# Optimization experiments

Hardware: AMD Instinct MI355X
Metric: run time of the kernel (lower is better)

The kernel has to match this reference:

```python
import jax, jax.numpy as jnp
import numpy as np

LMAX = 5
RESOLUTION = 12
ASPECT_RATIO = 2
BATCH = 256
NB = 2 * RESOLUTION                       # res_beta = 24
NA = round(2 * ASPECT_RATIO * RESOLUTION)  # res_alpha = res_gamma = 48
DIM = sum((2 * l + 1) ** 2 for l in range(LMAX + 1))  # 286

# normalize2mom constant for tanh: (E_{z~N(0,1)}[tanh(z)^2])^{-1/2}
_x = np.linspace(-12.0, 12.0, 1_000_001)
_pdf = np.exp(-0.5 * _x * _x) / np.sqrt(2.0 * np.pi)
ACT_CST = float(np.trapz(np.tanh(_x) ** 2 * _pdf, _x) ** -0.5)  # ~1.5927


def _su2_generators(j):
    m = np.arange(-j, j)
    raising = np.diag(-np.sqrt(j * (j + 1) - m * (m + 1)), k=-1).astype(complex)
    m = np.arange(-j + 1, j + 1)
    lowering = np.diag(np.sqrt(j * (j + 1) - m * (m - 1)), k=1).astype(complex)
    m = np.arange(-j, j + 1)
    return np.stack([0.5 * (raising + lowering), np.diag(1j * m), -0.5j * (raising - lowering)])


def _q_real_to_complex(l):
    q = np.zeros((2 * l + 1, 2 * l + 1), dtype=complex)
    for m in range(-l, 0):
        q[l + m, l + abs(m)] = 1 / np.sqrt(2)
        q[l + m, l - abs(m)] = -1j / np.sqrt(2)
    q[l, l] = 1
    for m in range(1, l + 1):
        q[l + m, l + abs(m)] = (-1) ** m / np.sqrt(2)
        q[l + m, l - abs(m)] = 1j * (-1) ** m / np.sqrt(2)
    return (-1j) ** l * q


def _so3_generators(l):
    X = _su2_generators(l)
    Q = _q_real_to_complex(l)
    return np.real(np.conj(Q.T)[None] @ X @ Q[None])  # real [3, 2l+1, 2l+1]


def _expm_angles(A, t):
    """exp(t_n * A) for real antisymmetric A via eigendecomposition. -> [n, d, d] real"""
    vals, vecs = np.linalg.eig(A.astype(complex))
    inv = np.linalg.inv(vecs)
    phases = np.exp(t[:, None] * vals[None, :])  # [n, d]
    return np.real(np.einsum('ij,nj,jk->nik', vecs, phases, inv))


def _build_D_and_qw():
    # Euler angle grids (e3nn SO3Grid convention)
    b = (np.arange(NB) + 0.5) / NB * np.pi          # beta   [nb]
    a = np.arange(NA) / NA * 2.0 * np.pi            # alpha=gamma [na]
    blocks = []
    for l in range(LMAX + 1):
        X = _so3_generators(l)
        Ra = _expm_angles(X[1], a)   # exp(alpha * X1)  [na,d,d]
        Rb = _expm_angles(X[0], b)   # exp(beta  * X0)  [nb,d,d]
        # D^l(a,b,c) = Ra[a] @ Rb[b] @ Ra[c]
        Dl = np.einsum('xij,yjk,zkl->xyzil', Ra, Rb, Ra)
        blocks.append(np.sqrt(2 * l + 1) * Dl.reshape(NA, NB, NA, -1))
    D = np.concatenate(blocks, axis=-1).astype(np.float32)  # [na, nb, na, dim]
    # lie_learn / Kostelec-Rockmore quadrature weights for beta
    bb = NB // 2
    k = np.arange(bb)
    j = np.arange(2 * bb)
    w = (2.0 / bb) * np.sin(np.pi * (2 * j + 1) / (4.0 * bb)) * np.sum(
        (1.0 / (2 * k + 1))[None, :]
        * np.sin((2 * j[:, None] + 1) * (2 * k[None, :] + 1) * np.pi / (4.0 * bb)),
        axis=1,
    )
    w = w / (2.0 * (2 * bb) ** 2)
    qw = (w * NB ** 2 / NA ** 2).astype(np.float32)  # [nb]
    return jnp.asarray(D), jnp.asarray(qw)


def setup_inputs() -> dict:
    key = jax.random.key(0)
    features = jax.random.normal(key, (BATCH, DIM), dtype=jnp.float32)
    D, qw = _build_D_and_qw()
    return {"features": features, "D": D, "qw": qw}


def reference(features, D, qw):
    dim = D.shape[-1]
    s = jnp.sqrt(jnp.asarray(dim, features.dtype))
    # to_grid: [B, dim] x [na, nb, na, dim] -> [B, na, nb, na]
    g = jnp.einsum('bi,xyzi->bxyz', features, D) / s
    # normalized pointwise nonlinearity on SO(3) samples
    g = ACT_CST * jnp.tanh(g)
    # from_grid: quadrature-weighted projection back onto flat Wigner basis
    return jnp.einsum('bxyz,y,xyzi->bi', g, qw, D) * s
```

## Files before the change

kernel.cpp:

```cpp
#include <hip/hip_runtime.h>
#include <hip/hip_bf16.h>

#define DIM    286
#define DIMP   288
#define NBATCH 256
#define NB_    24
#define NA_    48
#define ZC     32
#define NTILES 1728
#define NCHUNK 256
#define S_CONST 16.911534525287763f
#define INV_S   0.05913123959890826f
#define ACT_CST 1.5927f
#define TWO_LOG2E 2.8853900817779268f

typedef short bf16x8 __attribute__((ext_vector_type(8)));
typedef float f32x4  __attribute__((ext_vector_type(4)));

#define WS_FBF  0u
#define WS_PART 147456u

typedef const __attribute__((address_space(1))) char GA;
typedef __attribute__((address_space(3))) char LA;
__device__ __forceinline__ void gload_lds16(const void* g, void* l) {
    __builtin_amdgcn_global_load_lds((GA*)g, (LA*)l, 16, 0, 0);
}

__global__ void k_prepF(const float* __restrict__ F, __hip_bfloat16* __restrict__ Fbf) {
    int o = blockIdx.x * 256 + threadIdx.x;
    int row = o / DIMP, col = o % DIMP;
    float v = (col < DIM) ? F[row * DIM + col] * INV_S : 0.f;
    Fbf[o] = __float2bfloat16(v);
}

__launch_bounds__(512, 2)
__global__ void k_main(const __hip_bfloat16* __restrict__ Fbf,
                       const float* __restrict__ D,
                       const float* __restrict__ qw,
                       __hip_bfloat16* __restrict__ part) {
    __shared__ __align__(16) float Traw[2][9216];
    __shared__ __align__(16) char DsB[18432];
    __shared__ __align__(16) char DtB[18432];
    __shared__ __align__(16) char GsB[16384];
    __shared__ float qs[24];

    int t = threadIdx.x;
    int wave = t >> 6, lane = t & 63, ln = lane & 15, q = lane >> 4;
    int cA = (ln * 64 + q * 16) ^ ((ln & 7) << 4);
    int rq = ln * 64 + q * 16;
    int gA0 = (wave << 11) + (rq ^ ((ln >> 2) << 4));
    int gA1 = (wave << 11) + 1024 + (rq ^ ((4 + (ln >> 2)) << 4));

    if (t < 24) qs[t] = qw[t] * S_CONST;

    int rowbase = wave * 32;
    const __hip_bfloat16* fp0 = Fbf + (size_t)(rowbase + ln) * DIMP + q * 8;
    const __hip_bfloat16* fp1 = fp0 + 16 * DIMP;

    f32x4 acc[2][18];
    #pragma unroll
    for (int h = 0; h < 2; ++h)
        #pragma unroll
        for (int n = 0; n < 18; ++n) acc[h][n] = (f32x4){0.f, 0.f, 0.f, 0.f};

    int bx = blockIdx.x;
    int tstart = (bx < 192) ? bx * 7 : bx * 6 + 192;
    int ntile = (bx < 192) ? 7 : 6;

    int zseed = t / 144, iseed = t % 144;

    #define STAGE(TI, BUF) do {                                                    \
        const char* _s = (const char*)(D + (size_t)(tstart + (TI)) * 9152);        \
        char* _d = (char*)Traw[BUF];                                               \
        _Pragma("unroll")                                                          \
        for (int _j = 0; _j < 5; ++_j) {                                           \
            int _c = wave + _j * 8;                                                \
            if (_c < 35 || (_c == 35 && lane < 48))                                \
                gload_lds16(_s + _c * 1024 + lane * 16, _d + _c * 1024);           \
        }                                                                          \
    } while (0)

    STAGE(0, 0);
    STAGE(1, 1);
    asm volatile("s_waitcnt lgkmcnt(0)" ::: "memory");

    #pragma unroll 1
    for (int k = 0; k < ntile; ++k) {
        if (k + 1 < ntile) {
            if (wave < 4) asm volatile("s_waitcnt vmcnt(5)" ::: "memory");
            else          asm volatile("s_waitcnt vmcnt(4)" ::: "memory");
        } else {
            asm volatile("s_waitcnt vmcnt(0)" ::: "memory");
        }
        __builtin_amdgcn_s_barrier();

        const float* T = Traw[k & 1];
        {
            int zz = zseed, ii = iseed;
            #pragma unroll
            for (int m = 0; m < 9; ++m) {
                int i = ii * 2;
                __hip_bfloat162 o2;
                if (i < DIM) {
                    float2 v = *(const float2*)(&T[zz * DIM + i]);
                    o2.x = __float2bfloat16(v.x); o2.y = __float2bfloat16(v.y);
                } else {
                    o2.x = __float2bfloat16(0.f); o2.y = o2.x;
                }
                int off = (((i >> 5) * 2048) + zz * 64 + (i & 31) * 2) ^ ((zz & 7) << 4);
                *(__hip_bfloat162*)(DsB + off) = o2;
                zz += 3; ii += 80;
                if (ii >= 144) { ii -= 144; ++zz; }
            }
        }
        #pragma unroll
        for (int s5 = 0; s5 < 3; ++s5) {
            int idx = t + s5 * 512;
            if (idx < 1152) {
                int i = idx >> 2, zc = idx & 3;
                __hip_bfloat16 o8[8];
                #pragma unroll
                for (int j = 0; j < 8; ++j)
                    o8[j] = __float2bfloat16(T[(zc * 8 + j) * DIM + i]);
                int off = (i * 64 + zc * 16) ^ ((i & 7) << 4);
                *(bf16x8*)(DtB + off) = *(const bf16x8*)o8;
            }
        }
        asm volatile("s_waitcnt lgkmcnt(0)" ::: "memory");
        __builtin_amdgcn_s_barrier();

        if (k + 2 < ntile) STAGE(k + 2, k & 1);

        int z0t = (tstart + k) * 32;
        float qv0 = qs[((z0t + ln) / 48) % 24];
        float qv1 = qs[((z0t + 16 + ln) / 48) % 24];

        f32x4 g00 = (f32x4){0.f,0.f,0.f,0.f}, g01 = (f32x4){0.f,0.f,0.f,0.f};
        f32x4 g10 = (f32x4){0.f,0.f,0.f,0.f}, g11 = (f32x4){0.f,0.f,0.f,0.f};
        #pragma unroll 3
        for (int ks = 0; ks < 9; ++ks) {
            bf16x8 a0 = *(const bf16x8*)(fp0 + ks * 32);
            bf16x8 a1 = *(const bf16x8*)(fp1 + ks * 32);
            bf16x8 b0 = *(const bf16x8*)(DsB + ks * 2048 + cA);
            bf16x8 b1 = *(const bf16x8*)(DsB + ks * 2048 + 1024 + cA);
            g00 = __builtin_amdgcn_mfma_f32_16x16x32_bf16(a0, b0, g00, 0, 0, 0);
            g01 = __builtin_amdgcn_mfma_f32_16x16x32_bf16(a0, b1, g01, 0, 0, 0);
            g10 = __builtin_amdgcn_mfma_f32_16x16x32_bf16(a1, b0, g10, 0, 0, 0);
            g11 = __builtin_amdgcn_mfma_f32_16x16x32_bf16(a1, b1, g11, 0, 0, 0);
        }
        #pragma unroll
        for (int h = 0; h < 2; ++h) {
            #pragma unroll
            for (int zh = 0; zh < 2; ++zh) {
                f32x4 g = (h == 0) ? (zh == 0 ? g00 : g01) : (zh == 0 ? g10 : g11);
                float qv = (zh == 0) ? qv0 : qv1;
                #pragma unroll
                for (int r = 0; r < 4; ++r) {
                    float x = g[r];
                    float a = fabsf(x);
                    float e = __builtin_amdgcn_exp2f(-TWO_LOG2E * a);
                    float v = ACT_CST - 2.f * ACT_CST * e * __builtin_amdgcn_rcpf(1.f + e);
                    v = copysignf(v, x) * qv;
                    int row = h * 16 + q * 4 + r;
                    int goff = (wave << 11)
                             + ((row * 64 + (zh * 16 + ln) * 2) ^ ((row >> 2) << 4));
                    *(__hip_bfloat16*)(GsB + goff) = __float2bfloat16(v);
                }
            }
        }
        bf16x8 a20 = *(const bf16x8*)(GsB + gA0);
        bf16x8 a21 = *(const bf16x8*)(GsB + gA1);
        #pragma unroll
        for (int nf = 0; nf < 18; ++nf) {
            bf16x8 b2 = *(const bf16x8*)(DtB + nf * 1024 + cA);
            acc[0][nf] = __builtin_amdgcn_mfma_f32_16x16x32_bf16(a20, b2, acc[0][nf], 0, 0, 0);
            acc[1][nf] = __builtin_amdgcn_mfma_f32_16x16x32_bf16(a21, b2, acc[1][nf], 0, 0, 0);
        }
        __builtin_amdgcn_s_barrier();
    }
    #undef STAGE

    __hip_bfloat16* pw = part + (size_t)bx * (NBATCH * DIMP) + (size_t)rowbase * DIMP;
    #pragma unroll
    for (int h = 0; h < 2; ++h) {
        #pragma unroll
        for (int m = 0; m < 9; ++m) {
            __hip_bfloat16 o8[8];
            #pragma unroll
            for (int j = 0; j < 8; ++j)
                o8[j] = __float2bfloat16(acc[h][2 * m + (j >> 2)][j & 3]);
            *(bf16x8*)(pw + (size_t)((h * 9 + m) * 64 + lane) * 8) = *(const bf16x8*)o8;
        }
    }
}

__global__ void k_reduce(const __hip_bfloat16* __restrict__ part, float* __restrict__ out) {
    __shared__ float red[3][16][8];
    int t = threadIdx.x, wave = t >> 6, lane = t & 63;
    int j = lane & 15;
    int zg = wave * 4 + (lane >> 4);
    int s = blockIdx.x * 16 + j;
    const __hip_bfloat16* p = part + (size_t)s * 8;
    float sum[8];
    #pragma unroll
    for (int kk = 0; kk < 8; ++kk) sum[kk] = 0.f;
    #pragma unroll 4
    for (int ii = 0; ii < 16; ++ii) {
        bf16x8 v = *(const bf16x8*)(p + (size_t)(zg * 16 + ii) * (NBATCH * DIMP));
        #pragma unroll
        for (int kk = 0; kk < 8; ++kk) {
            __hip_bfloat16 h; *(short*)&h = v[kk];
            sum[kk] += __bfloat162float(h);
        }
    }
    #pragma unroll
    for (int kk = 0; kk < 8; ++kk) {
        sum[kk] += __shfl_down(sum[kk], 16);
        sum[kk] += __shfl_down(sum[kk], 32);
    }
    if (wave > 0 && lane < 16) {
        #pragma unroll
        for (int kk = 0; kk < 8; ++kk) red[wave - 1][lane][kk] = sum[kk];
    }
    __syncthreads();
    if (wave == 0 && lane < 16) {
        #pragma unroll
        for (int w = 0; w < 3; ++w)
            #pragma unroll
            for (int kk = 0; kk < 8; ++kk) sum[kk] += red[w][lane][kk];
        int wr = s / 1152, si = s % 1152;
        int lane_m = si % 64, m9 = si / 64;
        int h = m9 / 9, m = m9 % 9, q = lane_m >> 4, ln = lane_m & 15;
        int rowb = wr * 32 + h * 16 + q * 4;
        #pragma unroll
        for (int j8 = 0; j8 < 8; ++j8) {
            int nf = 2 * m + (j8 >> 2), r = j8 & 3;
            int i = nf * 16 + ln;
            if (i < DIM) out[(rowb + r) * DIM + i] = sum[j8];
        }
    }
}

extern "C" void kernel_launch(void* const* d_in, const int* in_sizes, int n_in,
                              void* d_out, int out_size, void* d_ws, size_t ws_size,
                              hipStream_t stream) {
    const float* F  = (const float*)d_in[0];
    const float* D  = (const float*)d_in[1];
    const float* qw = (const float*)d_in[2];
    char* ws = (char*)d_ws;
    __hip_bfloat16* Fbf = (__hip_bfloat16*)(ws + WS_FBF);
    __hip_bfloat16* part = (__hip_bfloat16*)(ws + WS_PART);

    k_prepF<<<288, 256, 0, stream>>>(F, Fbf);
    k_main<<<NCHUNK, 512, 0, stream>>>(Fbf, D, qw, part);
    k_reduce<<<576, 256, 0, stream>>>(part, (float*)d_out);
}
```

Baseline: 138.6 us.

## Fuse feature conversion into main kernel and run 16 waves per block

Removes the separate feature-to-bf16 prep kernel. Each wave now converts its own 16 feature rows directly from fp32 and keeps them in registers for the whole tile loop, instead of reloading bf16 rows from global memory every tile. Blocks grow from 512 to 1024 threads, so each wave owns 16 batch rows and half the accumulator tiles, and the staging and transpose work is spread over more threads. The intent is to drop one launch, cut repeated global loads and raise the number of waves hiding latency. In exchange, more waves share the same LDS and hit the same barriers, and register pressure is tighter under the new launch bounds.

```diff
diff --git a/kernel.cpp b/kernel.cpp
--- a/kernel.cpp
+++ b/kernel.cpp
@@ -17,8 +17,7 @@
 typedef short bf16x8 __attribute__((ext_vector_type(8)));
 typedef float f32x4  __attribute__((ext_vector_type(4)));
 
-#define WS_FBF  0u
-#define WS_PART 147456u
+#define WS_PART 0u
 
 typedef const __attribute__((address_space(1))) char GA;
 typedef __attribute__((address_space(3))) char LA;
@@ -26,15 +25,8 @@
     __builtin_amdgcn_global_load_lds((GA*)g, (LA*)l, 16, 0, 0);
 }
 
-__global__ void k_prepF(const float* __restrict__ F, __hip_bfloat16* __restrict__ Fbf) {
-    int o = blockIdx.x * 256 + threadIdx.x;
-    int row = o / DIMP, col = o % DIMP;
-    float v = (col < DIM) ? F[row * DIM + col] * INV_S : 0.f;
-    Fbf[o] = __float2bfloat16(v);
-}
-
-__launch_bounds__(512, 2)
-__global__ void k_main(const __hip_bfloat16* __restrict__ Fbf,
+__launch_bounds__(1024, 4)
+__global__ void k_main(const float* __restrict__ F,
                        const float* __restrict__ D,
                        const float* __restrict__ qw,
                        __hip_bfloat16* __restrict__ part) {
@@ -42,26 +34,35 @@
     __shared__ __align__(16) char DsB[18432];
     __shared__ __align__(16) char DtB[18432];
     __shared__ __align__(16) char GsB[16384];
-    __shared__ float qs[24];
+    float* qs = &Traw[0][9152];
 
     int t = threadIdx.x;
     int wave = t >> 6, lane = t & 63, ln = lane & 15, q = lane >> 4;
     int cA = (ln * 64 + q * 16) ^ ((ln & 7) << 4);
-    int rq = ln * 64 + q * 16;
-    int gA0 = (wave << 11) + (rq ^ ((ln >> 2) << 4));
-    int gA1 = (wave << 11) + 1024 + (rq ^ ((4 + (ln >> 2)) << 4));
+    int gA = (wave << 10) + ((ln * 64 + q * 16) ^ ((ln >> 2) << 4));
 
     if (t < 24) qs[t] = qw[t] * S_CONST;
 
-    int rowbase = wave * 32;
-    const __hip_bfloat16* fp0 = Fbf + (size_t)(rowbase + ln) * DIMP + q * 8;
-    const __hip_bfloat16* fp1 = fp0 + 16 * DIMP;
-
-    f32x4 acc[2][18];
-    #pragma unroll
-    for (int h = 0; h < 2; ++h)
-        #pragma unroll
-        for (int n = 0; n < 18; ++n) acc[h][n] = (f32x4){0.f, 0.f, 0.f, 0.f};
+    bf16x8 fa[9];
+    {
+        const float* Fr = F + (size_t)(wave * 16 + ln) * DIM + q * 8;
+        #pragma unroll
+        for (int ks = 0; ks < 9; ++ks) {
+            __hip_bfloat16 o[8];
+            #pragma unroll
+            for (int jj = 0; jj < 8; ++jj) {
+                int col = q * 8 + ks * 32 + jj;
+                float fv = 0.f;
+                if (col < DIM) fv = Fr[ks * 32 + jj];
+                o[jj] = __float2bfloat16(fv * INV_S);
+            }
+            fa[ks] = *(const bf16x8*)o;
+        }
+    }
+
+    f32x4 acc[18];
+    #pragma unroll
+    for (int n = 0; n < 18; ++n) acc[n] = (f32x4){0.f, 0.f, 0.f, 0.f};
 
     int bx = blockIdx.x;
     int tstart = (bx < 192) ? bx * 7 : bx * 6 + 192;
@@ -73,22 +74,22 @@
         const char* _s = (const char*)(D + (size_t)(tstart + (TI)) * 9152);        \
         char* _d = (char*)Traw[BUF];                                               \
         _Pragma("unroll")                                                          \
-        for (int _j = 0; _j < 5; ++_j) {                                           \
-            int _c = wave + _j * 8;                                                \
+        for (int _j = 0; _j < 3; ++_j) {                                           \
+            int _c = wave + _j * 16;                                               \
             if (_c < 35 || (_c == 35 && lane < 48))                                \
                 gload_lds16(_s + _c * 1024 + lane * 16, _d + _c * 1024);           \
         }                                                                          \
     } while (0)
 
+    asm volatile("s_waitcnt vmcnt(0) lgkmcnt(0)" ::: "memory");
     STAGE(0, 0);
     STAGE(1, 1);
-    asm volatile("s_waitcnt lgkmcnt(0)" ::: "memory");
 
     #pragma unroll 1
     for (int k = 0; k < ntile; ++k) {
         if (k + 1 < ntile) {
-            if (wave < 4) asm volatile("s_waitcnt vmcnt(5)" ::: "memory");
-            else          asm volatile("s_waitcnt vmcnt(4)" ::: "memory");
+            if (wave < 4) asm volatile("s_waitcnt vmcnt(3)" ::: "memory");
+            else          asm volatile("s_waitcnt vmcnt(2)" ::: "memory");
         } else {
             asm volatile("s_waitcnt vmcnt(0)" ::: "memory");
         }
@@ -98,33 +99,41 @@
         {
             int zz = zseed, ii = iseed;
             #pragma unroll
-            for (int m = 0; m < 9; ++m) {
-                int i = ii * 2;
-                __hip_bfloat162 o2;
-                if (i < DIM) {
-                    float2 v = *(const float2*)(&T[zz * DIM + i]);
-                    o2.x = __float2bfloat16(v.x); o2.y = __float2bfloat16(v.y);
-                } else {
-                    o2.x = __float2bfloat16(0.f); o2.y = o2.x;
+            for (int m = 0; m < 5; ++m) {
+                if (m < 4 || t < 512) {
+                    int i = ii * 2;
+                    __hip_bfloat162 o2;
+                    if (i < DIM) {
+                        float2 v = *(const float2*)(&T[zz * DIM + i]);
+                        o2.x = __float2bfloat16(v.x); o2.y = __float2bfloat16(v.y);
+                    } else {
+                        o2.x = __float2bfloat16(0.f); o2.y = o2.x;
+                    }
+                    int off = (((i >> 5) * 2048) + zz * 64 + (i & 31) * 2) ^ ((zz & 7) << 4);
+                    *(__hip_bfloat162*)(DsB + off) = o2;
                 }
-                int off = (((i >> 5) * 2048) + zz * 64 + (i & 31) * 2) ^ ((zz & 7) << 4);
-                *(__hip_bfloat162*)(DsB + off) = o2;
-                zz += 3; ii += 80;
+                zz += 7; ii += 16;
                 if (ii >= 144) { ii -= 144; ++zz; }
             }
         }
-        #pragma unroll
-        for (int s5 = 0; s5 < 3; ++s5) {
-            int idx = t + s5 * 512;
-            if (idx < 1152) {
-                int i = idx >> 2, zc = idx & 3;
-                __hip_bfloat16 o8[8];
-                #pragma unroll
-                for (int j = 0; j < 8; ++j)
-                    o8[j] = __float2bfloat16(T[(zc * 8 + j) * DIM + i]);
-                int off = (i * 64 + zc * 16) ^ ((i & 7) << 4);
-                *(bf16x8*)(DtB + off) = *(const bf16x8*)o8;
-            }
+        {
+            int i = t >> 2, zc = t & 3;
+            __hip_bfloat16 o8[8];
+            #pragma unroll
+            for (int j = 0; j < 8; ++j)
+                o8[j] = __float2bfloat16(T[(zc * 8 + j) * DIM + i]);
+            int off = (i * 64 + zc * 16) ^ ((i & 7) << 4);
+            *(bf16x8*)(DtB + off) = *(const bf16x8*)o8;
+        }
+        if (t < 128) {
+            int idx = 1024 + t;
+            int i = idx >> 2, zc = idx & 3;
+            __hip_bfloat16 o8[8];
+            #pragma unroll
+            for (int j = 0; j < 8; ++j)
+                o8[j] = __float2bfloat16(T[(zc * 8 + j) * DIM + i]);
+            int off = (i * 64 + zc * 16) ^ ((i & 7) << 4);
+            *(bf16x8*)(DtB + off) = *(const bf16x8*)o8;
         }
         asm volatile("s_waitcnt lgkmcnt(0)" ::: "memory");
         __builtin_amdgcn_s_barrier();
@@ -135,62 +144,51 @@
         float qv0 = qs[((z0t + ln) / 48) % 24];
         float qv1 = qs[((z0t + 16 + ln) / 48) % 24];
 
-        f32x4 g00 = (f32x4){0.f,0.f,0.f,0.f}, g01 = (f32x4){0.f,0.f,0.f,0.f};
-        f32x4 g10 = (f32x4){0.f,0.f,0.f,0.f}, g11 = (f32x4){0.f,0.f,0.f,0.f};
-        #pragma unroll 3
+        f32x4 g0 = (f32x4){0.f,0.f,0.f,0.f}, g1 = (f32x4){0.f,0.f,0.f,0.f};
+        #pragma unroll
         for (int ks = 0; ks < 9; ++ks) {
-            bf16x8 a0 = *(const bf16x8*)(fp0 + ks * 32);
-            bf16x8 a1 = *(const bf16x8*)(fp1 + ks * 32);
             bf16x8 b0 = *(const bf16x8*)(DsB + ks * 2048 + cA);
             bf16x8 b1 = *(const bf16x8*)(DsB + ks * 2048 + 1024 + cA);
-            g00 = __builtin_amdgcn_mfma_f32_16x16x32_bf16(a0, b0, g00, 0, 0, 0);
-            g01 = __builtin_amdgcn_mfma_f32_16x16x32_bf16(a0, b1, g01, 0, 0, 0);
-            g10 = __builtin_amdgcn_mfma_f32_16x16x32_bf16(a1, b0, g10, 0, 0, 0);
-            g11 = __builtin_amdgcn_mfma_f32_16x16x32_bf16(a1, b1, g11, 0, 0, 0);
-        }
-        #pragma unroll
-        for (int h = 0; h < 2; ++h) {
-            #pragma unroll
-            for (int zh = 0; zh < 2; ++zh) {
-                f32x4 g = (h == 0) ? (zh == 0 ? g00 : g01) : (zh == 0 ? g10 : g11);
-                float qv = (zh == 0) ? qv0 : qv1;
-                #pragma unroll
-                for (int r = 0; r < 4; ++r) {
-                    float x = g[r];
-                    float a = fabsf(x);
-                    float e = __builtin_amdgcn_exp2f(-TWO_LOG2E * a);
-                    float v = ACT_CST - 2.f * ACT_CST * e * __builtin_amdgcn_rcpf(1.f + e);
-                    v = copysignf(v, x) * qv;
-                    int row = h * 16 + q * 4 + r;
-                    int goff = (wave << 11)
-                             + ((row * 64 + (zh * 16 + ln) * 2) ^ ((row >> 2) << 4));
-                    *(__hip_bfloat16*)(GsB + goff) = __float2bfloat16(v);
-                }
+            g0 = __builtin_amdgcn_mfma_f32_16x16x32_bf16(fa[ks], b0, g0, 0, 0, 0);
+            g1 = __builtin_amdgcn_mfma_f32_16x16x32_bf16(fa[ks], b1, g1, 0, 0, 0);
+        }
+        #pragma unroll
+        for (int zh = 0; zh < 2; ++zh) {
+            f32x4 g = (zh == 0) ? g0 : g1;
+            float qv = (zh == 0) ? qv0 : qv1;
+            #pragma unroll
+            for (int r = 0; r < 4; ++r) {
+                float x = g[r];
+                float a = fabsf(x);
+                float e = __builtin_amdgcn_exp2f(-TWO_LOG2E * a);
+                float v = ACT_CST - 2.f * ACT_CST * e * __builtin_amdgcn_rcpf(1.f + e);
+                v = copysignf(v, x) * qv;
+                int row = q * 4 + r;
+                int goff = (wave << 10)
+                         + ((row * 64 + (zh * 16 + ln) * 2) ^ ((row >> 2) << 4));
+                *(__hip_bfloat16*)(GsB + goff) = __float2bfloat16(v);
             }
         }
-        bf16x8 a20 = *(const bf16x8*)(GsB + gA0);
-        bf16x8 a21 = *(const bf16x8*)(GsB + gA1);
+        bf16x8 a2 = *(const bf16x8*)(GsB + gA);
         #pragma unroll
         for (int nf = 0; nf < 18; ++nf) {
             bf16x8 b2 = *(const bf16x8*)(DtB + nf * 1024 + cA);
-            acc[0][nf] = __builtin_amdgcn_mfma_f32_16x16x32_bf16(a20, b2, acc[0][nf], 0, 0, 0);
-            acc[1][nf] = __builtin_amdgcn_mfma_f32_16x16x32_bf16(a21, b2, acc[1][nf], 0, 0, 0);
+            acc[nf] = __builtin_amdgcn_mfma_f32_16x16x32_bf16(a2, b2, acc[nf], 0, 0, 0);
         }
         __builtin_amdgcn_s_barrier();
     }
     #undef STAGE
 
-    __hip_bfloat16* pw = part + (size_t)bx * (NBATCH * DIMP) + (size_t)rowbase * DIMP;
-    #pragma unroll
-    for (int h = 0; h < 2; ++h) {
-        #pragma unroll
-        for (int m = 0; m < 9; ++m) {
-            __hip_bfloat16 o8[8];
-            #pragma unroll
-            for (int j = 0; j < 8; ++j)
-                o8[j] = __float2bfloat16(acc[h][2 * m + (j >> 2)][j & 3]);
-            *(bf16x8*)(pw + (size_t)((h * 9 + m) * 64 + lane) * 8) = *(const bf16x8*)o8;
-        }
+    int h = wave & 1;
+    __hip_bfloat16* pw = part + (size_t)bx * (NBATCH * DIMP)
+                       + (size_t)(wave >> 1) * 32 * DIMP;
+    #pragma unroll
+    for (int m = 0; m < 9; ++m) {
+        __hip_bfloat16 o8[8];
+        #pragma unroll
+        for (int j = 0; j < 8; ++j)
+            o8[j] = __float2bfloat16(acc[2 * m + (j >> 2)][j & 3]);
+        *(bf16x8*)(pw + (size_t)((h * 9 + m) * 64 + lane) * 8) = *(const bf16x8*)o8;
     }
 }
 
@@ -248,10 +246,8 @@
     const float* D  = (const float*)d_in[1];
     const float* qw = (const float*)d_in[2];
     char* ws = (char*)d_ws;
-    __hip_bfloat16* Fbf = (__hip_bfloat16*)(ws + WS_FBF);
     __hip_bfloat16* part = (__hip_bfloat16*)(ws + WS_PART);
 
-    k_prepF<<<288, 256, 0, stream>>>(F, Fbf);
-    k_main<<<NCHUNK, 512, 0, stream>>>(Fbf, D, qw, part);
+    k_main<<<NCHUNK, 1024, 0, stream>>>(F, D, qw, part);
     k_reduce<<<576, 256, 0, stream>>>(part, (float*)d_out);
 }
```

New measurement: 178.6 us. 1.29x slower.
